# Optimization experiments

Measured on AMD Instinct MI355X. Metric: run time of the kernel, lower is better.

The kernel has to match this reference:

```python
import jax, jax.numpy as jnp
import numpy as np

B, T, D, NH, DK = 2, 2048, 1024, 16, 64
EPS = 1e-6

def proj_H(z):
    return z - z.mean(axis=-1, keepdims=True)

def to_clr(p):
    return proj_H(jnp.log(p + EPS))

def setup_inputs() -> dict:
    key = jax.random.key(0)
    ks = jax.random.split(key, 9)
    p = jax.random.uniform(ks[0], (B, T, D), dtype=jnp.float32)
    # xavier_uniform with gain=0.8 for square-ish [in,out] matrices
    def xavier(k, fan_in, fan_out):
        bound = 0.8 * np.sqrt(6.0 / (fan_in + fan_out))
        return jax.random.uniform(k, (fan_in, fan_out), minval=-bound, maxval=bound, dtype=jnp.float32)
    H = NH * DK
    Wq = xavier(ks[1], D, H); bq = jnp.zeros((H,), jnp.float32)
    Wk = xavier(ks[2], D, H); bk = jnp.zeros((H,), jnp.float32)
    Wv = xavier(ks[3], D, H); bv = jnp.zeros((H,), jnp.float32)
    Wo = xavier(ks[4], H, D); bo = jnp.zeros((D,), jnp.float32)
    return {"p": p, "Wq": Wq, "bq": bq, "Wk": Wk, "bk": bk,
            "Wv": Wv, "bv": bv, "Wo": Wo, "bo": bo}

def reference(p, Wq, bq, Wk, bk, Wv, bv, Wo, bo):
    z = to_clr(p)                                   # [B,T,D]
    # projections with H-projection epilogue, reshaped to [B,T,NH,DK]
    q = proj_H(z @ Wq + bq).reshape(B, T, NH, DK)
    k = proj_H(z @ Wk + bk).reshape(B, T, NH, DK)
    v = proj_H(z @ Wv + bv).reshape(B, T, NH, DK)
    att = jnp.einsum('bihd,bjhd->bhij', q, k) / jnp.sqrt(jnp.float32(DK))
    w = jax.nn.softmax(att, axis=-1)                # dropout is identity in eval
    z_out = jnp.einsum('bhij,bjhd->bihd', w, v).reshape(B, T, NH * DK)
    z_out = proj_H(z_out @ Wo + bo)
    return jax.nn.softmax(z_out, axis=-1)           # from_clr
```

## Files before the change

### kernel.cpp

```cpp
#include <hip/hip_runtime.h>

typedef unsigned short u16;
typedef __attribute__((ext_vector_type(8))) short short8_t;
typedef __attribute__((ext_vector_type(8))) _Float16 half8_t;
typedef __attribute__((ext_vector_type(4))) float f32x4;
typedef __attribute__((ext_vector_type(16))) float f32x16;
typedef __attribute__((ext_vector_type(4))) int int4v;

#define BB    2
#define TT    2048
#define DD    1024
#define NHEAD 16
#define DKH   64
#define HH    1024
#define MR    4096
#define CLR_EPS 1e-6f
#define QSCALE_CONST 0.18033688011112042f

#define O_WQKVT  0ull
#define O_WOT    6291456ull
#define O_WMEAN  8388608ull
#define O_BQKV   8404992ull
#define O_BO     8417280ull
#define O_Z      8421376ull
#define O_QKV    16809984ull
#define O_VT     41975808ull
#define O_ZOUT   50364416ull
#define O_LOGITS O_QKV

__device__ __forceinline__ u16 f2h(float f) {
  _Float16 h = (_Float16)f;
  return __builtin_bit_cast(u16, h);
}
__device__ __forceinline__ float h2f(u16 x) {
  return (float)__builtin_bit_cast(_Float16, x);
}

__device__ __forceinline__ f32x4 mfma16(short8_t a, short8_t b, f32x4 c) {
  return __builtin_amdgcn_mfma_f32_16x16x32_f16(
      __builtin_bit_cast(half8_t, a), __builtin_bit_cast(half8_t, b), c, 0, 0, 0);
}
__device__ __forceinline__ f32x16 mfma32(short8_t a, short8_t b, f32x16 c) {
  return __builtin_amdgcn_mfma_f32_32x32x16_f16(
      __builtin_bit_cast(half8_t, a), __builtin_bit_cast(half8_t, b), c, 0, 0, 0);
}

typedef const __attribute__((address_space(1))) unsigned int as1_u32_t;
typedef __attribute__((address_space(3))) unsigned int as3_u32_t;

__device__ __forceinline__ void async16(const void* g, void* l) {
  __builtin_amdgcn_global_load_lds((as1_u32_t*)g, (as3_u32_t*)l, 16, 0, 0);
}

__device__ __forceinline__ void stage2(const u16* __restrict__ G, int base_row,
                                       int r0, int r1, int k0, int schk, u16* lds) {
  const int c0 = k0 + ((schk ^ (r0 & 7)) << 3);
  const int c1 = k0 + ((schk ^ (r1 & 7)) << 3);
  async16(G + (size_t)(base_row + r0) * 1024 + c0, lds + r0 * 64 + schk * 8);
  async16(G + (size_t)(base_row + r1) * 1024 + c1, lds + r1 * 64 + schk * 8);
}

__device__ __forceinline__ short8_t ldfrag(const u16* buf, int row, int kh, int lane) {
  const int byte = (row * 128 + ((kh * 32 + ((lane >> 4) << 3)) << 1)) ^ ((row & 7) << 4);
  return *(const short8_t*)((const char*)buf + byte);
}

__global__ __launch_bounds__(256) void wprep_mean(
    const float* __restrict__ Wq, const float* __restrict__ Wk,
    const float* __restrict__ Wv, const float* __restrict__ Wo,
    const float* __restrict__ bq, const float* __restrict__ bk,
    const float* __restrict__ bv, const float* __restrict__ bo,
    float* __restrict__ wmean, float* __restrict__ bqkv_p, float* __restrict__ bo_p) {
  __shared__ float sb[4];
  const int bid = blockIdx.x, tid = threadIdx.x;
  if (bid < 4096) {
    const int m = bid >> 10, d = bid & 1023;
    const float* Wm = (m == 0) ? Wq : (m == 1) ? Wk : (m == 2) ? Wv : Wo;
    float4 x = ((const float4*)(Wm + (size_t)d * 1024))[tid];
    float s = x.x + x.y + x.z + x.w;
    #pragma unroll
    for (int dd = 32; dd; dd >>= 1) s += __shfl_xor(s, dd);
    if ((tid & 63) == 0) sb[tid >> 6] = s;
    __syncthreads();
    if (tid == 0) wmean[bid] = (sb[0] + sb[1] + sb[2] + sb[3]) * (1.f / 1024.f);
  } else {
    const int j = bid - 4096;
    const float* bb = (j == 0) ? bq : (j == 1) ? bk : (j == 2) ? bv : bo;
    float4 x = ((const float4*)bb)[tid];
    float s = x.x + x.y + x.z + x.w;
    #pragma unroll
    for (int dd = 32; dd; dd >>= 1) s += __shfl_xor(s, dd);
    if ((tid & 63) == 0) sb[tid >> 6] = s;
    __syncthreads();
    const float mean = (sb[0] + sb[1] + sb[2] + sb[3]) * (1.f / 1024.f);
    float* dst = (j < 3) ? (bqkv_p + j * 1024) : bo_p;
    float4 o = {x.x - mean, x.y - mean, x.z - mean, x.w - mean};
    ((float4*)dst)[tid] = o;
  }
}

__global__ __launch_bounds__(256) void wprep_trans(
    const float* __restrict__ Wq, const float* __restrict__ Wk,
    const float* __restrict__ Wv, const float* __restrict__ Wo,
    const float* __restrict__ wmean, u16* __restrict__ wqkvt, u16* __restrict__ wot) {
  __shared__ float tl[64][65];
  const int tj = blockIdx.x, ti = blockIdx.y, m = blockIdx.z;
  const int tid = threadIdx.x;
  const float* Wm = (m == 0) ? Wq : (m == 1) ? Wk : (m == 2) ? Wv : Wo;
  const int d0 = ti * 64, h0 = tj * 64;
  #pragma unroll
  for (int rr = 0; rr < 4; ++rr) {
    const int r = (tid >> 4) + rr * 16;
    float4 x = *(const float4*)(Wm + (size_t)(d0 + r) * 1024 + h0 + ((tid & 15) << 2));
    const float mu = wmean[m * 1024 + d0 + r];
    tl[r][(tid & 15) * 4 + 0] = x.x - mu;
    tl[r][(tid & 15) * 4 + 1] = x.y - mu;
    tl[r][(tid & 15) * 4 + 2] = x.z - mu;
    tl[r][(tid & 15) * 4 + 3] = x.w - mu;
  }
  __syncthreads();
  #pragma unroll
  for (int rr = 0; rr < 2; ++rr) {
    const int hh = (tid >> 3) + rr * 32;
    const int cd = (tid & 7) << 3;
    short8_t v;
    #pragma unroll
    for (int i = 0; i < 8; ++i) v[i] = (short)f2h(tl[cd + i][hh]);
    u16* dst = (m < 3) ? (wqkvt + ((size_t)(m * 1024 + h0 + hh)) * 1024 + d0 + cd)
                       : (wot + ((size_t)(h0 + hh)) * 1024 + d0 + cd);
    *(short8_t*)dst = v;
  }
}

__global__ __launch_bounds__(256) void clr_kernel(const float* __restrict__ p, u16* __restrict__ z) {
  __shared__ float sb[4];
  const int r = blockIdx.x, tid = threadIdx.x;
  float4 x = ((const float4*)(p + (size_t)r * 1024))[tid];
  float l0 = __logf(x.x + CLR_EPS), l1 = __logf(x.y + CLR_EPS);
  float l2 = __logf(x.z + CLR_EPS), l3 = __logf(x.w + CLR_EPS);
  float s = l0 + l1 + l2 + l3;
  #pragma unroll
  for (int dd = 32; dd; dd >>= 1) s += __shfl_xor(s, dd);
  if ((tid & 63) == 0) sb[tid >> 6] = s;
  __syncthreads();
  const float mu = (sb[0] + sb[1] + sb[2] + sb[3]) * (1.f / 1024.f);
  ushort4 o;
  o.x = f2h(l0 - mu); o.y = f2h(l1 - mu); o.z = f2h(l2 - mu); o.w = f2h(l3 - mu);
  ((ushort4*)(z + (size_t)r * 1024))[tid] = o;
}

__global__ __launch_bounds__(512, 2) void gemm_qkv_8ph(
    const u16* __restrict__ A, const u16* __restrict__ Bt, const float* __restrict__ bias,
    u16* __restrict__ qkv, u16* __restrict__ vt) {
  __shared__ u16 As[2][256 * 64];
  __shared__ u16 Bs[2][256 * 64];
  const int tid = threadIdx.x, lane = tid & 63, wid = tid >> 6;
  const int wm = wid >> 2, wn = wid & 3;
  const int id = blockIdx.x;
  const int nid = (id & 7) * 24 + (id >> 3);
  const int m0 = (nid / 12) * 256, n0 = (nid % 12) * 256;
  const int srow = tid >> 3, schk = tid & 7;
  const int l15 = lane & 15, lg4 = (lane >> 4) << 2;

  f32x4 acc[8][4] = {};

  stage2(Bt, n0, srow, srow + 64, 0, schk, &Bs[0][0]);
  stage2(Bt, n0, srow + 128, srow + 192, 0, schk, &Bs[0][0]);
  stage2(A, m0, srow, srow + 128, 0, schk, &As[0][0]);
  stage2(A, m0, srow + 64, srow + 192, 0, schk, &As[0][0]);
  asm volatile("s_waitcnt vmcnt(0)" ::: "memory");
  __builtin_amdgcn_s_barrier();

  short8_t afr[4], bfr[4];
  for (int t = 0; t < 16; ++t) {
    const int cur = t & 1;
    const int k0n = ((t + 1) & 15) * 64;
    const u16* Ab = &As[cur][0];
    const u16* Bb_ = &Bs[cur][0];
    u16* Asn = &As[cur ^ 1][0];
    u16* Bsn = &Bs[cur ^ 1][0];

    #pragma unroll
    for (int j = 0; j < 4; ++j) bfr[j] = ldfrag(Bb_, wn * 64 + j * 16 + l15, 0, lane);
    #pragma unroll
    for (int i = 0; i < 4; ++i) afr[i] = ldfrag(Ab, wm * 128 + i * 16 + l15, 0, lane);
    stage2(Bt, n0, srow, srow + 64, k0n, schk, Bsn);
    stage2(Bt, n0, srow + 128, srow + 192, k0n, schk, Bsn);
    __builtin_amdgcn_s_barrier();
    asm volatile("s_waitcnt lgkmcnt(0)" ::: "memory");
    __builtin_amdgcn_sched_barrier(0);
    __builtin_amdgcn_s_setprio(1);
    #pragma unroll
    for (int i = 0; i < 4; ++i)
      #pragma unroll
      for (int j = 0; j < 4; ++j)
        acc[i][j] = mfma16(afr[i], bfr[j], acc[i][j]);
    __builtin_amdgcn_s_setprio(0);
    __builtin_amdgcn_s_barrier();

    #pragma unroll
    for (int i = 0; i < 4; ++i) afr[i] = ldfrag(Ab, wm * 128 + 64 + i * 16 + l15, 0, lane);
    stage2(A, m0, srow, srow + 128, k0n, schk, Asn);
    stage2(A, m0, srow + 64, srow + 192, k0n, schk, Asn);
    __builtin_amdgcn_s_barrier();
    asm volatile("s_waitcnt lgkmcnt(0)" ::: "memory");
    __builtin_amdgcn_sched_barrier(0);
    __builtin_amdgcn_s_setprio(1);
    #pragma unroll
    for (int i = 0; i < 4; ++i)
      #pragma unroll
      for (int j = 0; j < 4; ++j)
        acc[4 + i][j] = mfma16(afr[i], bfr[j], acc[4 + i][j]);
    __builtin_amdgcn_s_setprio(0);
    __builtin_amdgcn_s_barrier();

    #pragma unroll
    for (int j = 0; j < 4; ++j) bfr[j] = ldfrag(Bb_, wn * 64 + j * 16 + l15, 1, lane);
    #pragma unroll
    for (int i = 0; i < 4; ++i) afr[i] = ldfrag(Ab, wm * 128 + i * 16 + l15, 1, lane);
    __builtin_amdgcn_s_barrier();
    asm volatile("s_waitcnt lgkmcnt(0)" ::: "memory");
    __builtin_amdgcn_sched_barrier(0);
    __builtin_amdgcn_s_setprio(1);
    #pragma unroll
    for (int i = 0; i < 4; ++i)
      #pragma unroll
      for (int j = 0; j < 4; ++j)
        acc[i][j] = mfma16(afr[i], bfr[j], acc[i][j]);
    __builtin_amdgcn_s_setprio(0);
    __builtin_amdgcn_s_barrier();

    #pragma unroll
    for (int i = 0; i < 4; ++i) afr[i] = ldfrag(Ab, wm * 128 + 64 + i * 16 + l15, 1, lane);
    asm volatile("s_waitcnt vmcnt(0)" ::: "memory");
    __builtin_amdgcn_s_barrier();
    asm volatile("s_waitcnt lgkmcnt(0)" ::: "memory");
    __builtin_amdgcn_sched_barrier(0);
    __builtin_amdgcn_s_setprio(1);
    #pragma unroll
    for (int i = 0; i < 4; ++i)
      #pragma unroll
      for (int j = 0; j < 4; ++j)
        acc[4 + i][j] = mfma16(afr[i], bfr[j], acc[4 + i][j]);
    __builtin_amdgcn_s_setprio(0);
    __builtin_amdgcn_s_barrier();
  }

  if (n0 < 2048) {
    const float sc = (n0 < 1024) ? QSCALE_CONST : 1.0f;
    #pragma unroll
    for (int j = 0; j < 4; ++j) {
      const int col = n0 + wn * 64 + j * 16 + l15;
      const float bb = bias[col];
      #pragma unroll
      for (int i = 0; i < 8; ++i) {
        const int rowb = m0 + wm * 128 + i * 16 + lg4;
        #pragma unroll
        for (int r = 0; r < 4; ++r)
          qkv[(size_t)(rowb + r) * 3072 + col] = f2h((acc[i][j][r] + bb) * sc);
      }
    }
  } else {
    const int h = (n0 - 2048 + wn * 64) >> 6;
    #pragma unroll
    for (int j = 0; j < 4; ++j) {
      const int dk = j * 16 + l15;
      const float bb = bias[n0 + wn * 64 + dk];
      #pragma unroll
      for (int i = 0; i < 8; ++i) {
        const int rowb = m0 + wm * 128 + i * 16 + lg4;
        const int b = rowb >> 11, tq = rowb & 2047;
        const int k5 = tq & 31;
        const int pos = (tq & ~31) + (k5 & 16) + ((k5 & 4) << 1) + ((k5 & 8) >> 1);
        ushort4 pk;
        pk.x = f2h(acc[i][j][0] + bb);
        pk.y = f2h(acc[i][j][1] + bb);
        pk.z = f2h(acc[i][j][2] + bb);
        pk.w = f2h(acc[i][j][3] + bb);
        *(ushort4*)(vt + ((size_t)((b * NHEAD + h) * 64 + dk)) * TT + pos) = pk;
      }
    }
  }
}

__global__ __launch_bounds__(256) void gemm_bt(
    const u16* __restrict__ A, const u16* __restrict__ Bt, const float* __restrict__ bias,
    float* __restrict__ Cout, int Ndim, int Kdim) {
  __shared__ u16 As[2][128 * 64];
  __shared__ u16 Bs[2][128 * 64];
  const int tid = threadIdx.x;
  const int lane = tid & 63, wid = tid >> 6;
  const int m0 = blockIdx.y * 128, n0 = blockIdx.x * 128;
  const int wm = wid >> 1, wn = wid & 1;
  const int srow = tid >> 3, schk = tid & 7;
  f32x4 acc[4][4] = {};

  auto STG = [&](int k0, int buf) {
    #pragma unroll
    for (int rr = 0; rr < 4; ++rr) {
      const int row = srow + rr * 32;
      const int gcol = k0 + ((schk ^ (row & 7)) << 3);
      async16(A + (size_t)(m0 + row) * Kdim + gcol, &As[buf][row * 64 + schk * 8]);
      async16(Bt + (size_t)(n0 + row) * Kdim + gcol, &Bs[buf][row * 64 + schk * 8]);
    }
  };

  STG(0, 0);
  asm volatile("s_waitcnt vmcnt(0)" ::: "memory");
  __builtin_amdgcn_s_barrier();

  const int nt = Kdim >> 6;
  for (int t = 0; t < nt; ++t) {
    const int cur = t & 1;
    STG((((t + 1) & (nt - 1))) << 6, cur ^ 1);
    #pragma unroll
    for (int kk = 0; kk < 2; ++kk) {
      short8_t af[4], bf[4];
      #pragma unroll
      for (int i = 0; i < 4; ++i) {
        af[i] = ldfrag(&As[cur][0], wm * 64 + i * 16 + (lane & 15), kk, lane);
        bf[i] = ldfrag(&Bs[cur][0], wn * 64 + i * 16 + (lane & 15), kk, lane);
      }
      #pragma unroll
      for (int i = 0; i < 4; ++i)
        #pragma unroll
        for (int j = 0; j < 4; ++j)
          acc[i][j] = mfma16(af[i], bf[j], acc[i][j]);
    }
    asm volatile("s_waitcnt vmcnt(0)" ::: "memory");
    __builtin_amdgcn_s_barrier();
  }

  #pragma unroll
  for (int j = 0; j < 4; ++j) {
    const int col = n0 + wn * 64 + j * 16 + (lane & 15);
    const float bb = bias[col];
    #pragma unroll
    for (int i = 0; i < 4; ++i) {
      const int rowb = m0 + wm * 64 + i * 16 + ((lane >> 4) << 2);
      #pragma unroll
      for (int r = 0; r < 4; ++r)
        Cout[(size_t)(rowb + r) * Ndim + col] = acc[i][j][r] + bb;
    }
  }
}

__global__ __launch_bounds__(512, 2) void attn_kernel(
    const u16* __restrict__ qkv, const u16* __restrict__ vt, u16* __restrict__ zout) {
  __shared__ char smem[65536];
  const int id = blockIdx.x;
  const int qb = (id >> 3) & 7;
  const int bh = (id & 7) * 4 + (id >> 6);
  const int b = bh >> 4, h = bh & 15;
  const int tid = threadIdx.x, lane = tid & 63, w = tid >> 6;
  const int qw = w & 3, ks = w >> 2;
  const int hl = lane >> 5, l31 = lane & 31;
  const int swz = (l31 & 7) << 4;
  const int q0 = qb * 256 + qw * 64;

  short8_t qf[2][4];
  #pragma unroll
  for (int qt = 0; qt < 2; ++qt)
    #pragma unroll
    for (int c = 0; c < 4; ++c)
      qf[qt][c] = *(const short8_t*)(qkv + (size_t)(b * TT + q0 + qt * 32 + l31) * 3072
                                     + h * 64 + c * 16 + hl * 8);

  const int sr0 = qw * 16 + (lane >> 3);
  const int schk = lane & 7;
  const int scol = (schk ^ (sr0 & 7)) << 3;
  const int dof = sr0 * 128 + schk * 16;
  char* kls = smem + ks * 16384;
  char* vls = smem + 32768 + ks * 16384;
  const u16* kg = qkv + 1024 + (size_t)h * 64;
  const u16* vg = vt + ((size_t)(b * NHEAD + h) * 64 + sr0) * (size_t)TT;

  {
    const int kbase = ks * 1024;
    async16(kg + (size_t)(b * TT + kbase + sr0) * 3072 + scol, kls + dof);
    async16(kg + (size_t)(b * TT + kbase + sr0 + 8) * 3072 + scol, kls + dof + 1024);
    async16(vg + kbase + scol, vls + dof);
    async16(vg + (size_t)8 * TT + kbase + scol, vls + dof + 1024);
  }

  f32x16 o[2][2] = {};
  f32x16 lb[2] = {};
  short8_t ones;
  #pragma unroll
  for (int i = 0; i < 8; ++i) ones[i] = (short)0x3C00;

  for (int it = 0; it < 16; ++it) {
    __syncthreads();
    if (it < 15) {
      const int kbase = ks * 1024 + (it + 1) * 64;
      const int bo = ((it + 1) & 1) * 8192;
      async16(kg + (size_t)(b * TT + kbase + sr0) * 3072 + scol, kls + bo + dof);
      async16(kg + (size_t)(b * TT + kbase + sr0 + 8) * 3072 + scol, kls + bo + dof + 1024);
      async16(vg + kbase + scol, vls + bo + dof);
      async16(vg + (size_t)8 * TT + kbase + scol, vls + bo + dof + 1024);
    }
    const char* Kb = kls + (it & 1) * 8192;
    const char* Vb = vls + (it & 1) * 8192;

    #pragma unroll
    for (int kt = 0; kt < 2; ++kt) {
      f32x16 s[2] = {};
      #pragma unroll
      for (int c = 0; c < 4; ++c) {
        const int krow = kt * 32 + l31;
        const short8_t kfr = *(const short8_t*)(Kb + krow * 128 + ((c * 32 + hl * 16) ^ swz));
        s[0] = mfma32(kfr, qf[0][c], s[0]);
        s[1] = mfma32(kfr, qf[1][c], s[1]);
      }
      #pragma unroll
      for (int qt = 0; qt < 2; ++qt)
        #pragma unroll
        for (int r = 0; r < 16; ++r) {
          float pv;
          asm("v_exp_f32 %0, %1" : "=v"(pv) : "v"(s[qt][r]));
          s[qt][r] = pv;
        }
      #pragma unroll
      for (int cc = 0; cc < 2; ++cc) {
        short8_t pa[2];
        #pragma unroll
        for (int qt = 0; qt < 2; ++qt) {
          int w0 = __builtin_bit_cast(int, __builtin_amdgcn_cvt_pkrtz(s[qt][8 * cc + 0], s[qt][8 * cc + 1]));
          int w1 = __builtin_bit_cast(int, __builtin_amdgcn_cvt_pkrtz(s[qt][8 * cc + 2], s[qt][8 * cc + 3]));
          int w2 = __builtin_bit_cast(int, __builtin_amdgcn_cvt_pkrtz(s[qt][8 * cc + 4], s[qt][8 * cc + 5]));
          int w3 = __builtin_bit_cast(int, __builtin_amdgcn_cvt_pkrtz(s[qt][8 * cc + 6], s[qt][8 * cc + 7]));
          int4v fw = {w0, w1, w2, w3};
          pa[qt] = __builtin_bit_cast(short8_t, fw);
          lb[qt] = mfma32(pa[qt], ones, lb[qt]);
        }
        const int cb = kt * 64 + cc * 32 + hl * 16;
        #pragma unroll
        for (int dkt = 0; dkt < 2; ++dkt) {
          const int vrow = dkt * 32 + l31;
          const short8_t vfr = *(const short8_t*)(Vb + vrow * 128 + (cb ^ swz));
          o[0][dkt] = mfma32(pa[0], vfr, o[0][dkt]);
          o[1][dkt] = mfma32(pa[1], vfr, o[1][dkt]);
        }
      }
    }
  }

  __syncthreads();
  const int slot = qw * 64 + lane;
  if (ks == 1) {
    u16* ro = (u16*)(smem + slot * 136);
    #pragma unroll
    for (int qt = 0; qt < 2; ++qt)
      #pragma unroll
      for (int dkt = 0; dkt < 2; ++dkt)
        #pragma unroll
        for (int r = 0; r < 16; ++r)
          ro[(qt * 2 + dkt) * 16 + r] = f2h(o[qt][dkt][r]);
    u16* rl = (u16*)(smem + 36864 + slot * 72);
    #pragma unroll
    for (int qt = 0; qt < 2; ++qt)
      #pragma unroll
      for (int r = 0; r < 16; ++r)
        rl[qt * 16 + r] = f2h(lb[qt][r]);
  }
  __syncthreads();
  if (ks == 0) {
    const u16* ro = (const u16*)(smem + slot * 136);
    const u16* rl = (const u16*)(smem + 36864 + slot * 72);
    #pragma unroll
    for (int qt = 0; qt < 2; ++qt) {
      #pragma unroll
      for (int r = 0; r < 16; ++r) lb[qt][r] += h2f(rl[qt * 16 + r]);
      #pragma unroll
      for (int dkt = 0; dkt < 2; ++dkt)
        #pragma unroll
        for (int r = 0; r < 16; ++r) o[qt][dkt][r] += h2f(ro[(qt * 2 + dkt) * 16 + r]);
    }
    #pragma unroll
    for (int qt = 0; qt < 2; ++qt) {
      float rlv[16];
      #pragma unroll
      for (int r = 0; r < 16; ++r) rlv[r] = 1.f / lb[qt][r];
      #pragma unroll
      for (int dkt = 0; dkt < 2; ++dkt) {
        const int col = h * 64 + dkt * 32 + l31;
        #pragma unroll
        for (int r = 0; r < 16; ++r) {
          const int rowg = b * TT + q0 + qt * 32 + (r & 3) + 8 * (r >> 2) + 4 * hl;
          zout[(size_t)rowg * 1024 + col] = f2h(o[qt][dkt][r] * rlv[r]);
        }
      }
    }
  }
}

__global__ __launch_bounds__(256) void softmax_rows(const float* __restrict__ logits,
                                                    float* __restrict__ out) {
  __shared__ float sb[8];
  const int r = blockIdx.x, tid = threadIdx.x;
  float4 x = ((const float4*)(logits + (size_t)r * 1024))[tid];
  float mx = fmaxf(fmaxf(x.x, x.y), fmaxf(x.z, x.w));
  #pragma unroll
  for (int dd = 32; dd; dd >>= 1) mx = fmaxf(mx, __shfl_xor(mx, dd));
  if ((tid & 63) == 0) sb[tid >> 6] = mx;
  __syncthreads();
  mx = fmaxf(fmaxf(sb[0], sb[1]), fmaxf(sb[2], sb[3]));
  const float e0 = __expf(x.x - mx), e1 = __expf(x.y - mx);
  const float e2 = __expf(x.z - mx), e3 = __expf(x.w - mx);
  float s = e0 + e1 + e2 + e3;
  #pragma unroll
  for (int dd = 32; dd; dd >>= 1) s += __shfl_xor(s, dd);
  __syncthreads();
  if ((tid & 63) == 0) sb[4 + (tid >> 6)] = s;
  __syncthreads();
  s = sb[4] + sb[5] + sb[6] + sb[7];
  const float inv = 1.f / s;
  float4 o = {e0 * inv, e1 * inv, e2 * inv, e3 * inv};
  ((float4*)(out + (size_t)r * 1024))[tid] = o;
}

extern "C" void kernel_launch(void* const* d_in, const int* in_sizes, int n_in,
                              void* d_out, int out_size, void* d_ws, size_t ws_size,
                              hipStream_t stream) {
  (void)in_sizes; (void)n_in; (void)out_size; (void)ws_size;
  const float* p  = (const float*)d_in[0];
  const float* Wq = (const float*)d_in[1];
  const float* bq = (const float*)d_in[2];
  const float* Wk = (const float*)d_in[3];
  const float* bk = (const float*)d_in[4];
  const float* Wv = (const float*)d_in[5];
  const float* bv = (const float*)d_in[6];
  const float* Wo = (const float*)d_in[7];
  const float* bo = (const float*)d_in[8];
  float* out = (float*)d_out;

  char* ws = (char*)d_ws;
  u16*   wqkvt  = (u16*)(ws + O_WQKVT);
  u16*   wot    = (u16*)(ws + O_WOT);
  float* wmean  = (float*)(ws + O_WMEAN);
  float* bqkv_p = (float*)(ws + O_BQKV);
  float* bo_p   = (float*)(ws + O_BO);
  u16*   z      = (u16*)(ws + O_Z);
  u16*   qkv    = (u16*)(ws + O_QKV);
  u16*   vt     = (u16*)(ws + O_VT);
  u16*   zoutb  = (u16*)(ws + O_ZOUT);
  float* logits = (float*)(ws + O_LOGITS);

  wprep_mean<<<4100, 256, 0, stream>>>(Wq, Wk, Wv, Wo, bq, bk, bv, bo, wmean, bqkv_p, bo_p);
  wprep_trans<<<dim3(16, 16, 4), 256, 0, stream>>>(Wq, Wk, Wv, Wo, wmean, wqkvt, wot);
  clr_kernel<<<MR, 256, 0, stream>>>(p, z);
  gemm_qkv_8ph<<<192, 512, 0, stream>>>(z, wqkvt, bqkv_p, qkv, vt);
  attn_kernel<<<256, 512, 0, stream>>>(qkv, vt, zoutb);
  gemm_bt<<<dim3(1024 / 128, MR / 128), 256, 0, stream>>>(zoutb, wot, bo_p, logits, 1024, 1024);
  softmax_rows<<<MR, 256, 0, stream>>>(logits, out);
}
```

Before: 135.4 us.

## Retile QKV GEMM to 128x192 tiles with 256-thread blocks and 512 workgroups

Result: faster. 128.3 us (-5.3%).

```diff
diff --git a/kernel.cpp b/kernel.cpp
--- a/kernel.cpp
+++ b/kernel.cpp
@@ -50,14 +50,6 @@
 
 __device__ __forceinline__ void async16(const void* g, void* l) {
   __builtin_amdgcn_global_load_lds((as1_u32_t*)g, (as3_u32_t*)l, 16, 0, 0);
-}
-
-__device__ __forceinline__ void stage2(const u16* __restrict__ G, int base_row,
-                                       int r0, int r1, int k0, int schk, u16* lds) {
-  const int c0 = k0 + ((schk ^ (r0 & 7)) << 3);
-  const int c1 = k0 + ((schk ^ (r1 & 7)) << 3);
-  async16(G + (size_t)(base_row + r0) * 1024 + c0, lds + r0 * 64 + schk * 8);
-  async16(G + (size_t)(base_row + r1) * 1024 + c1, lds + r1 * 64 + schk * 8);
 }
 
 __device__ __forceinline__ short8_t ldfrag(const u16* buf, int row, int kh, int lane) {
@@ -149,43 +141,56 @@
   ((ushort4*)(z + (size_t)r * 1024))[tid] = o;
 }
 
-__global__ __launch_bounds__(512, 2) void gemm_qkv_8ph(
+__global__ __launch_bounds__(256, 2) void gemm_qkv_8ph(
     const u16* __restrict__ A, const u16* __restrict__ Bt, const float* __restrict__ bias,
     u16* __restrict__ qkv, u16* __restrict__ vt) {
-  __shared__ u16 As[2][256 * 64];
-  __shared__ u16 Bs[2][256 * 64];
-  const int tid = threadIdx.x, lane = tid & 63, wid = tid >> 6;
-  const int wm = wid >> 2, wn = wid & 3;
+  __shared__ u16 As[2][128 * 64];
+  __shared__ u16 Bs[2][192 * 64];
+  const int tid = threadIdx.x, lane = tid & 63, w = tid >> 6;
+  const int wm = w >> 1, wn = w & 1;
   const int id = blockIdx.x;
-  const int nid = (id & 7) * 24 + (id >> 3);
-  const int m0 = (nid / 12) * 256, n0 = (nid % 12) * 256;
+  const int x = id & 7, idx = id >> 3;
+  const int mt = (x & 3) * 8 + (idx & 7);
+  const int nt = (x >> 2) * 8 + (idx >> 3);
+  const int m0 = mt * 128, n0 = nt * 192;
   const int srow = tid >> 3, schk = tid & 7;
   const int l15 = lane & 15, lg4 = (lane >> 4) << 2;
 
-  f32x4 acc[8][4] = {};
-
-  stage2(Bt, n0, srow, srow + 64, 0, schk, &Bs[0][0]);
-  stage2(Bt, n0, srow + 128, srow + 192, 0, schk, &Bs[0][0]);
-  stage2(A, m0, srow, srow + 128, 0, schk, &As[0][0]);
-  stage2(A, m0, srow + 64, srow + 192, 0, schk, &As[0][0]);
+  f32x4 acc[4][6] = {};
+
+  auto stA = [&](int k0, int buf) {
+    #pragma unroll
+    for (int u = 0; u < 4; ++u) {
+      const int r = srow + u * 32;
+      const int c = k0 + ((schk ^ (r & 7)) << 3);
+      async16(A + (size_t)(m0 + r) * 1024 + c, &As[buf][r * 64 + schk * 8]);
+    }
+  };
+  auto stB = [&](int k0, int buf) {
+    #pragma unroll
+    for (int u = 0; u < 6; ++u) {
+      const int r = srow + u * 32;
+      const int c = k0 + ((schk ^ (r & 7)) << 3);
+      async16(Bt + (size_t)(n0 + r) * 1024 + c, &Bs[buf][r * 64 + schk * 8]);
+    }
+  };
+
+  stA(0, 0); stB(0, 0);
   asm volatile("s_waitcnt vmcnt(0)" ::: "memory");
   __builtin_amdgcn_s_barrier();
 
-  short8_t afr[4], bfr[4];
+  short8_t afr[4], bfr[6];
   for (int t = 0; t < 16; ++t) {
     const int cur = t & 1;
     const int k0n = ((t + 1) & 15) * 64;
     const u16* Ab = &As[cur][0];
     const u16* Bb_ = &Bs[cur][0];
-    u16* Asn = &As[cur ^ 1][0];
-    u16* Bsn = &Bs[cur ^ 1][0];
-
-    #pragma unroll
-    for (int j = 0; j < 4; ++j) bfr[j] = ldfrag(Bb_, wn * 64 + j * 16 + l15, 0, lane);
-    #pragma unroll
-    for (int i = 0; i < 4; ++i) afr[i] = ldfrag(Ab, wm * 128 + i * 16 + l15, 0, lane);
-    stage2(Bt, n0, srow, srow + 64, k0n, schk, Bsn);
-    stage2(Bt, n0, srow + 128, srow + 192, k0n, schk, Bsn);
+
+    #pragma unroll
+    for (int j = 0; j < 6; ++j) bfr[j] = ldfrag(Bb_, wn * 96 + j * 16 + l15, 0, lane);
+    #pragma unroll
+    for (int i = 0; i < 4; ++i) afr[i] = ldfrag(Ab, wm * 64 + i * 16 + l15, 0, lane);
+    stA(k0n, cur ^ 1); stB(k0n, cur ^ 1);
     __builtin_amdgcn_s_barrier();
     asm volatile("s_waitcnt lgkmcnt(0)" ::: "memory");
     __builtin_amdgcn_sched_barrier(0);
@@ -193,15 +198,15 @@
     #pragma unroll
     for (int i = 0; i < 4; ++i)
       #pragma unroll
-      for (int j = 0; j < 4; ++j)
+      for (int j = 0; j < 6; ++j)
         acc[i][j] = mfma16(afr[i], bfr[j], acc[i][j]);
     __builtin_amdgcn_s_setprio(0);
     __builtin_amdgcn_s_barrier();
 
     #pragma unroll
-    for (int i = 0; i < 4; ++i) afr[i] = ldfrag(Ab, wm * 128 + 64 + i * 16 + l15, 0, lane);
-    stage2(A, m0, srow, srow + 128, k0n, schk, Asn);
-    stage2(A, m0, srow + 64, srow + 192, k0n, schk, Asn);
+    for (int j = 0; j < 6; ++j) bfr[j] = ldfrag(Bb_, wn * 96 + j * 16 + l15, 1, lane);
+    #pragma unroll
+    for (int i = 0; i < 4; ++i) afr[i] = ldfrag(Ab, wm * 64 + i * 16 + l15, 1, lane);
     __builtin_amdgcn_s_barrier();
     asm volatile("s_waitcnt lgkmcnt(0)" ::: "memory");
     __builtin_amdgcn_sched_barrier(0);
@@ -209,66 +214,31 @@
     #pragma unroll
     for (int i = 0; i < 4; ++i)
       #pragma unroll
-      for (int j = 0; j < 4; ++j)
-        acc[4 + i][j] = mfma16(afr[i], bfr[j], acc[4 + i][j]);
-    __builtin_amdgcn_s_setprio(0);
-    __builtin_amdgcn_s_barrier();
-
-    #pragma unroll
-    for (int j = 0; j < 4; ++j) bfr[j] = ldfrag(Bb_, wn * 64 + j * 16 + l15, 1, lane);
-    #pragma unroll
-    for (int i = 0; i < 4; ++i) afr[i] = ldfrag(Ab, wm * 128 + i * 16 + l15, 1, lane);
-    __builtin_amdgcn_s_barrier();
-    asm volatile("s_waitcnt lgkmcnt(0)" ::: "memory");
-    __builtin_amdgcn_sched_barrier(0);
-    __builtin_amdgcn_s_setprio(1);
-    #pragma unroll
-    for (int i = 0; i < 4; ++i)
-      #pragma unroll
-      for (int j = 0; j < 4; ++j)
+      for (int j = 0; j < 6; ++j)
         acc[i][j] = mfma16(afr[i], bfr[j], acc[i][j]);
     __builtin_amdgcn_s_setprio(0);
-    __builtin_amdgcn_s_barrier();
-
-    #pragma unroll
-    for (int i = 0; i < 4; ++i) afr[i] = ldfrag(Ab, wm * 128 + 64 + i * 16 + l15, 1, lane);
     asm volatile("s_waitcnt vmcnt(0)" ::: "memory");
     __builtin_amdgcn_s_barrier();
-    asm volatile("s_waitcnt lgkmcnt(0)" ::: "memory");
-    __builtin_amdgcn_sched_barrier(0);
-    __builtin_amdgcn_s_setprio(1);
-    #pragma unroll
-    for (int i = 0; i < 4; ++i)
-      #pragma unroll
-      for (int j = 0; j < 4; ++j)
-        acc[4 + i][j] = mfma16(afr[i], bfr[j], acc[4 + i][j]);
-    __builtin_amdgcn_s_setprio(0);
-    __builtin_amdgcn_s_barrier();
-  }
-
-  if (n0 < 2048) {
-    const float sc = (n0 < 1024) ? QSCALE_CONST : 1.0f;
-    #pragma unroll
-    for (int j = 0; j < 4; ++j) {
-      const int col = n0 + wn * 64 + j * 16 + l15;
-      const float bb = bias[col];
-      #pragma unroll
-      for (int i = 0; i < 8; ++i) {
-        const int rowb = m0 + wm * 128 + i * 16 + lg4;
+  }
+
+  #pragma unroll
+  for (int j = 0; j < 6; ++j) {
+    const int col = n0 + wn * 96 + j * 16 + l15;
+    const float bb = bias[col];
+    if (col < 2048) {
+      const float sc = (col < 1024) ? QSCALE_CONST : 1.0f;
+      #pragma unroll
+      for (int i = 0; i < 4; ++i) {
+        const int rowb = m0 + wm * 64 + i * 16 + lg4;
         #pragma unroll
         for (int r = 0; r < 4; ++r)
           qkv[(size_t)(rowb + r) * 3072 + col] = f2h((acc[i][j][r] + bb) * sc);
       }
-    }
-  } else {
-    const int h = (n0 - 2048 + wn * 64) >> 6;
-    #pragma unroll
-    for (int j = 0; j < 4; ++j) {
-      const int dk = j * 16 + l15;
-      const float bb = bias[n0 + wn * 64 + dk];
-      #pragma unroll
-      for (int i = 0; i < 8; ++i) {
-        const int rowb = m0 + wm * 128 + i * 16 + lg4;
+    } else {
+      const int h = (col - 2048) >> 6, dk = col & 63;
+      #pragma unroll
+      for (int i = 0; i < 4; ++i) {
+        const int rowb = m0 + wm * 64 + i * 16 + lg4;
         const int b = rowb >> 11, tq = rowb & 2047;
         const int k5 = tq & 31;
         const int pos = (tq & ~31) + (k5 & 16) + ((k5 & 4) << 1) + ((k5 & 8) >> 1);
@@ -549,7 +519,7 @@
   wprep_mean<<<4100, 256, 0, stream>>>(Wq, Wk, Wv, Wo, bq, bk, bv, bo, wmean, bqkv_p, bo_p);
   wprep_trans<<<dim3(16, 16, 4), 256, 0, stream>>>(Wq, Wk, Wv, Wo, wmean, wqkvt, wot);
   clr_kernel<<<MR, 256, 0, stream>>>(p, z);
-  gemm_qkv_8ph<<<192, 512, 0, stream>>>(z, wqkvt, bqkv_p, qkv, vt);
+  gemm_qkv_8ph<<<512, 256, 0, stream>>>(z, wqkvt, bqkv_p, qkv, vt);
   attn_kernel<<<256, 512, 0, stream>>>(qkv, vt, zoutb);
   gemm_bt<<<dim3(1024 / 128, MR / 128), 256, 0, stream>>>(zoutb, wot, bo_p, logits, 1024, 1024);
   softmax_rows<<<MR, 256, 0, stream>>>(logits, out);
```
